# Kernel tuning notes

Hardware: AMD Instinct MI355X
Metric: run time of the kernel (lower is better)

## Reference

```python
import jax, jax.numpy as jnp
import numpy as np

N_HEADS = 16


def _apply_rope(x, cos, sin):
    # x: [B, H, S, hd]; cos/sin: [>=S, hd/2]
    S = x.shape[2]
    cos = cos[None, None, :S]
    sin = sin[None, None, :S]
    x1, x2 = x[..., ::2], x[..., 1::2]
    # interleaved rotate, matching torch stack(...).flatten(-2)
    return jnp.stack([x1 * cos - x2 * sin, x1 * sin + x2 * cos], axis=-1).reshape(x.shape)


def setup_inputs() -> dict:
    key = jax.random.key(0)
    B, S, D = 2, 2048, 1024
    hd = D // N_HEADS
    k1, k2, k3 = jax.random.split(key, 3)
    x = jax.random.normal(k1, (B, S, D), dtype=jnp.float32)
    # standard RoPE tables (theta=10000)
    inv_freq = 1.0 / (10000.0 ** (np.arange(0, hd, 2, dtype=np.float32) / hd))  # [hd/2]
    freqs = np.outer(np.arange(S, dtype=np.float32), inv_freq)  # [S, hd/2]
    rope_cos = jnp.asarray(np.cos(freqs), dtype=jnp.float32)
    rope_sin = jnp.asarray(np.sin(freqs), dtype=jnp.float32)
    W_qkv = jax.random.normal(k2, (D, 3 * D), dtype=jnp.float32) * (D ** -0.5)
    W_out = jax.random.normal(k3, (D, D), dtype=jnp.float32) * (D ** -0.5)
    return {"x": x, "rope_cos": rope_cos, "rope_sin": rope_sin, "W_qkv": W_qkv, "W_out": W_out}


def reference(x, rope_cos, rope_sin, W_qkv, W_out):
    B, S, D = x.shape
    H = N_HEADS
    hd = D // H
    qkv = (x @ W_qkv).reshape(B, S, 3, H, hd)  # fused QKV projection
    q = qkv[:, :, 0].transpose(0, 2, 1, 3)  # [B,H,S,hd]
    k = qkv[:, :, 1].transpose(0, 2, 1, 3)
    v = qkv[:, :, 2].transpose(0, 2, 1, 3)
    q = _apply_rope(q, rope_cos, rope_sin)
    k = _apply_rope(k, rope_cos, rope_sin)
    scale = hd ** -0.5
    scores = jnp.einsum('bhqd,bhkd->bhqk', q, k) * scale  # [B,H,S,S]
    causal = jnp.tril(jnp.ones((S, S), dtype=bool))
    scores = jnp.where(causal, scores, jnp.finfo(scores.dtype).min)
    attn = jax.nn.softmax(scores, axis=-1)
    out = jnp.einsum('bhqk,bhkd->bhqd', attn, v)  # [B,H,S,hd]
    out = out.transpose(0, 2, 1, 3).reshape(B, S, D)
    return out @ W_out  # dropout is identity in eval mode
```

## Files before the change

kernel.cpp:

```cpp
#include <hip/hip_runtime.h>
#include <hip/hip_bf16.h>
#include <stdint.h>

typedef short bf16x8 __attribute__((ext_vector_type(8)));
typedef short bf16x4 __attribute__((ext_vector_type(4)));
typedef float f32x4 __attribute__((ext_vector_type(4)));

#define HD 64
#define NH 16
#define SEQ 2048
#define BATCH 2
#define DM 1024
#define TOK (BATCH * SEQ)

__device__ __forceinline__ unsigned short f2bf(float f) {
    union { float f; unsigned u; } a; a.f = f;
    unsigned r = a.u + 0x7fffu + ((a.u >> 16) & 1u);
    return (unsigned short)(r >> 16);
}
__device__ __forceinline__ float bf2f(unsigned short u) {
    union { unsigned u; float f; } a; a.u = ((unsigned)u) << 16;
    return a.f;
}

__device__ __forceinline__ unsigned pkbf16(float a, float b) {
    union { __hip_bfloat162 h; unsigned u; } cv;
    cv.h = __float22bfloat162_rn(make_float2(a, b));
    return cv.u;
}

__device__ __forceinline__ float fexp2(float x) {
#if __has_builtin(__builtin_amdgcn_exp2f)
    return __builtin_amdgcn_exp2f(x);
#else
    return exp2f(x);
#endif
}
__device__ __forceinline__ float frcp(float x) {
#if __has_builtin(__builtin_amdgcn_rcpf)
    return __builtin_amdgcn_rcpf(x);
#else
    return 1.0f / x;
#endif
}

__device__ __forceinline__ f32x4 mfma16(bf16x4 a, bf16x4 b, f32x4 c) {
#if defined(__HIP_DEVICE_COMPILE__)
    return __builtin_amdgcn_mfma_f32_16x16x16bf16_1k(a, b, c, 0, 0, 0);
#else
    (void)a; (void)b;
    return c;
#endif
}

__device__ __forceinline__ void gld_lds16(const unsigned short* g, unsigned short* l) {
#if __has_builtin(__builtin_amdgcn_global_load_lds)
    __builtin_amdgcn_global_load_lds(
        (const __attribute__((address_space(1))) unsigned int*)g,
        (__attribute__((address_space(3))) unsigned int*)l, 16, 0, 0);
#else
    *(bf16x8*)l = *(const bf16x8*)g;
#endif
}

__global__ void __launch_bounds__(256) k_prep(const float* __restrict__ x,
                                              unsigned short* __restrict__ xb,
                                              const float* __restrict__ wqkv,
                                              unsigned short* __restrict__ wqkvt,
                                              const float* __restrict__ wout,
                                              unsigned short* __restrict__ woutt) {
    int bid = blockIdx.x;
    int tid = threadIdx.x;
    if (bid < 4096) {
        int i = (bid * 256 + tid) * 4;
        float4 v = *(const float4*)(x + i);
        union { ushort4 v; unsigned short s[4]; } o;
        o.s[0] = f2bf(v.x); o.s[1] = f2bf(v.y); o.s[2] = f2bf(v.z); o.s[3] = f2bf(v.w);
        *(ushort4*)(xb + i) = o.v;
        return;
    }
    const float* W; unsigned short* Wt; int N, t;
    if (bid < 7168) { W = wqkv; Wt = wqkvt; N = 3 * DM; t = bid - 4096; }
    else            { W = wout; Wt = woutt; N = DM;     t = bid - 7168; }
    int ntx = N >> 5;
    int bx = t % ntx, by = t / ntx;
    int tx = tid & 31, ty = tid >> 5;
    __shared__ float tile[32][33];
    for (int r = 0; r < 4; ++r) {
        int k = by * 32 + ty + r * 8;
        int n = bx * 32 + tx;
        tile[ty + r * 8][tx] = W[(size_t)k * N + n];
    }
    __syncthreads();
    for (int r = 0; r < 4; ++r) {
        int n = bx * 32 + ty + r * 8;
        int k = by * 32 + tx;
        Wt[(size_t)n * DM + k] = f2bf(tile[tx][ty + r * 8]);
    }
}

#define BKK 32

template <int MODE>
__device__ __forceinline__ void gemm_core(const unsigned short* __restrict__ A,
                                          const unsigned short* __restrict__ Bt,
                                          int K, int N,
                                          float* __restrict__ C,
                                          unsigned short* __restrict__ qbuf,
                                          unsigned short* __restrict__ kbuf,
                                          unsigned short* __restrict__ vt) {
    __shared__ unsigned short As0[128 * BKK];
    __shared__ unsigned short As1[128 * BKK];
    __shared__ unsigned short Bs0[128 * BKK];
    __shared__ unsigned short Bs1[128 * BKK];
    int tid = threadIdx.x;
    int lane = tid & 63, wave = tid >> 6;
    int row0 = blockIdx.y * 128;
    int col0 = blockIdx.x * 128;
    int wm = (wave >> 1) * 64, wn = (wave & 1) * 64;
    int fr = lane & 15;
    int quad = lane >> 4;

    f32x4 zero4 = {0.f, 0.f, 0.f, 0.f};
    f32x4 acc[4][4];
    for (int i = 0; i < 4; ++i)
        for (int j = 0; j < 4; ++j) acc[i][j] = zero4;

    auto stage = [&](unsigned short* Ad, unsigned short* Bd, int k0) {
        for (int i = 0; i < 2; ++i) {
            int s2 = i * 256 + tid;
            int r = s2 >> 2, kc = s2 & 3;
            int kk = (kc ^ (r & 3)) * 8;
            gld_lds16(A + (size_t)(row0 + r) * K + k0 + kk, Ad + (i * 256 + wave * 64) * 8);
            gld_lds16(Bt + (size_t)(col0 + r) * K + k0 + kk, Bd + (i * 256 + wave * 64) * 8);
        }
    };
    auto compute = [&](const unsigned short* Al, const unsigned short* Bl) {
        bf16x8 af[4], bf[4];
        for (int i = 0; i < 4; ++i) {
            int rr = wm + i * 16 + fr;
            af[i] = *(const bf16x8*)&Al[rr * BKK + ((quad ^ (rr & 3)) * 8)];
        }
        for (int j = 0; j < 4; ++j) {
            int rr = wn + j * 16 + fr;
            bf[j] = *(const bf16x8*)&Bl[rr * BKK + ((quad ^ (rr & 3)) * 8)];
        }
        for (int i = 0; i < 4; ++i)
            for (int j = 0; j < 4; ++j)
                acc[i][j] = __builtin_amdgcn_mfma_f32_16x16x32_bf16(af[i], bf[j], acc[i][j], 0, 0, 0);
    };

    stage(As0, Bs0, 0);
    __syncthreads();
    for (int k0 = 0; k0 < K; k0 += 2 * BKK) {
        if (k0 + BKK < K) stage(As1, Bs1, k0 + BKK);
        compute(As0, Bs0);
        __syncthreads();
        if (k0 + 2 * BKK < K) stage(As0, Bs0, k0 + 2 * BKK);
        compute(As1, Bs1);
        __syncthreads();
    }

    int rq = (lane >> 4) * 4;
    int cq = lane & 15;
    for (int i = 0; i < 4; ++i)
        for (int j = 0; j < 4; ++j)
            for (int reg = 0; reg < 4; ++reg) {
                int row = row0 + wm + i * 16 + rq + reg;
                int col = col0 + wn + j * 16 + cq;
                float v = acc[i][j][reg];
                if (MODE == 0) {
                    C[(size_t)row * N + col] = v;
                } else {
                    int which = col >> 10;
                    int hc = col & 1023;
                    int h = hc >> 6, d = hc & 63;
                    int b = row >> 11, s = row & (SEQ - 1);
                    int bh = b * NH + h;
                    unsigned short bv = f2bf(v);
                    if (which == 0)      qbuf[((size_t)bh * SEQ + s) * HD + d] = bv;
                    else if (which == 1) kbuf[((size_t)bh * SEQ + s) * HD + d] = bv;
                    else                 vt[((size_t)bh * HD + d) * SEQ + s] = bv;
                }
            }
}

__global__ void __launch_bounds__(256) k_gemm_qkv(const unsigned short* __restrict__ A,
                                                  const unsigned short* __restrict__ Bt,
                                                  unsigned short* __restrict__ qbuf,
                                                  unsigned short* __restrict__ kbuf,
                                                  unsigned short* __restrict__ vt) {
    gemm_core<1>(A, Bt, DM, 3 * DM, nullptr, qbuf, kbuf, vt);
}

__global__ void __launch_bounds__(256) k_gemm_out(const unsigned short* __restrict__ A,
                                                  const unsigned short* __restrict__ Bt,
                                                  float* __restrict__ C) {
    gemm_core<0>(A, Bt, DM, DM, C, nullptr, nullptr, nullptr);
}

__global__ void k_rope(unsigned short* __restrict__ qbuf, unsigned short* __restrict__ kbuf,
                       const float* __restrict__ cosb, const float* __restrict__ sinb) {
    int t = blockIdx.x * 256 + threadIdx.x;
    int c = t & 7;
    int row = (t >> 3) & 65535;
    int which = t >> 19;
    unsigned short* p = (which ? kbuf : qbuf) + (size_t)row * HD + c * 8;
    float sc = which ? 1.0f : (0.125f * 1.44269504f);
    int s = row & (SEQ - 1);
    const float* cs = cosb + s * 32 + c * 4;
    const float* sn = sinb + s * 32 + c * 4;
    bf16x8 v = *(const bf16x8*)p;
    bf16x8 o;
    for (int i = 0; i < 4; ++i) {
        float x1 = bf2f((unsigned short)v[2 * i]);
        float x2 = bf2f((unsigned short)v[2 * i + 1]);
        float cc = cs[i], ss = sn[i];
        o[2 * i]     = (short)f2bf((x1 * cc - x2 * ss) * sc);
        o[2 * i + 1] = (short)f2bf((x1 * ss + x2 * cc) * sc);
    }
    *(bf16x8*)p = o;
}

__global__ void __launch_bounds__(128, 2) k_attn(const unsigned short* __restrict__ qbuf,
                                                 const unsigned short* __restrict__ kbuf,
                                                 const unsigned short* __restrict__ vt,
                                                 unsigned short* __restrict__ obuf) {
    __shared__ unsigned short Ks0[64 * 64];
    __shared__ unsigned short Ks1[64 * 64];
    __shared__ unsigned short Vs0[64 * 64];
    __shared__ unsigned short Vs1[64 * 64];

    int tid = threadIdx.x;
    int lane = tid & 63, wave = tid >> 6;
    int bh = blockIdx.y;
    int b = bh >> 4, h = bh & 15;
    int p = ((int)blockIdx.x + (int)blockIdx.y) & 31;
    int fr = lane & 15, quad = lane >> 4, sw = fr & 7;
    int Qb0 = (2 * p + wave) * 16;
    int Qb1 = (127 - 2 * p - wave) * 16;
    int KT = ((127 - 2 * p) >> 2) + 1;

    const unsigned short* Qb = qbuf + (size_t)bh * SEQ * HD;
    const unsigned short* Kb = kbuf + (size_t)bh * SEQ * HD;
    const unsigned short* Vb = vt + (size_t)bh * HD * SEQ;

    bf16x8 qf[2][2];
    for (int s = 0; s < 2; ++s) {
        int qrow = (s ? Qb1 : Qb0) + fr;
        qf[s][0] = *(const bf16x8*)(Qb + (size_t)qrow * HD + quad * 8);
        qf[s][1] = *(const bf16x8*)(Qb + (size_t)qrow * HD + 32 + quad * 8);
    }

    f32x4 zero4 = {0.f, 0.f, 0.f, 0.f};
    f32x4 o[2][4];
    for (int s = 0; s < 2; ++s)
        for (int j = 0; j < 4; ++j) o[s][j] = zero4;
    float l[2] = {0.f, 0.f};

    auto stage = [&](int kb, unsigned short* Kd, unsigned short* Vd) {
        for (int a = 0; a < 4; ++a) {
            int idx = a * 128 + tid;
            int r = idx >> 3;
            int lg = (idx & 7) ^ (r & 7);
            gld_lds16(Kb + (size_t)(kb + r) * HD + lg * 8, Kd + (a * 128 + wave * 64) * 8);
            gld_lds16(Vb + (size_t)r * SEQ + kb + lg * 8, Vd + (a * 128 + wave * 64) * 8);
        }
    };

    auto compute = [&](int kt, const unsigned short* Kd, const unsigned short* Vd) {
        int kb = kt * 64;
        bf16x8 ka[4], kc[4];
        for (int g = 0; g < 4; ++g) {
            int r = g * 16 + fr;
            ka[g] = *(const bf16x8*)&Kd[r * 64 + ((quad ^ sw) * 8)];
            kc[g] = *(const bf16x8*)&Kd[r * 64 + (((quad + 4) ^ sw) * 8)];
        }
        bf16x4 vf[4][4];
        for (int g = 0; g < 4; ++g)
            for (int db = 0; db < 4; ++db) {
                int d = db * 16 + fr;
                int pg = ((2 * g + (quad >> 1)) ^ sw) * 8 + (quad & 1) * 4;
                vf[g][db] = *(const bf16x4*)&Vd[d * 64 + pg];
            }
        for (int s = 0; s < 2; ++s) {
            int Qs = s ? Qb1 : Qb0;
            if (kb > Qs + 15) continue;
            f32x4 sg[4];
            for (int g = 0; g < 4; ++g) {
                f32x4 z = zero4;
                z = __builtin_amdgcn_mfma_f32_16x16x32_bf16(ka[g], qf[s][0], z, 0, 0, 0);
                z = __builtin_amdgcn_mfma_f32_16x16x32_bf16(kc[g], qf[s][1], z, 0, 0, 0);
                sg[g] = z;
            }
            if (kb + 63 > Qs) {
                int q = Qs + fr;
                for (int g = 0; g < 4; ++g)
                    for (int reg = 0; reg < 4; ++reg)
                        if (kb + g * 16 + quad * 4 + reg > q) sg[g][reg] = -1e30f;
            }
            bf16x4 pf[4];
            for (int g = 0; g < 4; ++g) {
                float p0 = fexp2(sg[g][0]);
                float p1 = fexp2(sg[g][1]);
                float p2 = fexp2(sg[g][2]);
                float p3 = fexp2(sg[g][3]);
                l[s] += (p0 + p1) + (p2 + p3);
                union { bf16x4 v; unsigned u[2]; } pc;
                pc.u[0] = pkbf16(p0, p1);
                pc.u[1] = pkbf16(p2, p3);
                pf[g] = pc.v;
            }
            for (int g = 0; g < 4; ++g)
                for (int db = 0; db < 4; ++db)
                    o[s][db] = mfma16(pf[g], vf[g][db], o[s][db]);
        }
    };

    stage(0, Ks0, Vs0);
    __syncthreads();
    for (int kt = 0; kt < KT; kt += 2) {
        if (kt + 1 < KT) stage((kt + 1) * 64, Ks1, Vs1);
        compute(kt, Ks0, Vs0);
        __syncthreads();
        if (kt + 1 < KT) {
            if (kt + 2 < KT) stage((kt + 2) * 64, Ks0, Vs0);
            compute(kt + 1, Ks1, Vs1);
            __syncthreads();
        }
    }

    for (int s = 0; s < 2; ++s) {
        float ll = l[s];
        ll += __shfl_xor(ll, 16);
        ll += __shfl_xor(ll, 32);
        float linv[4];
        for (int reg = 0; reg < 4; ++reg)
            linv[reg] = frcp(__shfl(ll, quad * 4 + reg));
        int Qs = s ? Qb1 : Qb0;
        for (int db = 0; db < 4; ++db)
            for (int reg = 0; reg < 4; ++reg) {
                int row = Qs + quad * 4 + reg;
                int d = db * 16 + fr;
                obuf[((size_t)(b * SEQ + row)) * DM + h * HD + d] = f2bf(o[s][db][reg] * linv[reg]);
            }
    }
}

extern "C" void kernel_launch(void* const* d_in, const int* in_sizes, int n_in,
                              void* d_out, int out_size, void* d_ws, size_t ws_size,
                              hipStream_t stream) {
    const float* x    = (const float*)d_in[0];
    const float* rc   = (const float*)d_in[1];
    const float* rs   = (const float*)d_in[2];
    const float* wqkv = (const float*)d_in[3];
    const float* wout = (const float*)d_in[4];
    float* out = (float*)d_out;

    char* ws = (char*)d_ws;
    size_t off = 0;
    auto alloc = [&](size_t bytes) {
        char* p = ws + off;
        off += (bytes + 255) & ~(size_t)255;
        return p;
    };
    unsigned short* xb    = (unsigned short*)alloc((size_t)TOK * DM * 2);
    unsigned short* wqkvt = (unsigned short*)alloc((size_t)3 * DM * DM * 2);
    unsigned short* woutt = (unsigned short*)alloc((size_t)DM * DM * 2);
    unsigned short* qbuf  = (unsigned short*)alloc((size_t)BATCH * NH * SEQ * HD * 2);
    unsigned short* kbuf  = (unsigned short*)alloc((size_t)BATCH * NH * SEQ * HD * 2);
    unsigned short* vtb   = (unsigned short*)alloc((size_t)BATCH * NH * SEQ * HD * 2);
    unsigned short* obuf  = (unsigned short*)alloc((size_t)TOK * DM * 2);

    k_prep<<<8192, 256, 0, stream>>>(x, xb, wqkv, wqkvt, wout, woutt);
    k_gemm_qkv<<<dim3(3 * DM / 128, TOK / 128), 256, 0, stream>>>(xb, wqkvt, qbuf, kbuf, vtb);
    k_rope<<<4096, 256, 0, stream>>>(qbuf, kbuf, rc, rs);
    k_attn<<<dim3(SEQ / 64, BATCH * NH), 128, 0, stream>>>(qbuf, kbuf, vtb, obuf);
    k_gemm_out<<<dim3(DM / 128, TOK / 128), 256, 0, stream>>>(obuf, woutt, out);
}
```

Baseline: 183.4 us.

## Rewrite QKV GEMM with 256x256 tiles, triple-buffered direct-to-LDS loads and swizzled grid

Replaces the generic 128x128 QKV projection GEMM with a dedicated kernel that uses 256x256 output tiles, 512 threads (8 waves, each computing a 128x64 sub-tile) and a three-slot LDS ring fed by global-to-LDS loads with XOR-swizzled columns. Block indices are remapped so neighbouring blocks share input rows and columns in cache. MFMA issue runs at raised wave priority. The aim is more data reuse per loaded byte, loads that overlap compute, and a grid of 192 blocks that fits the CU count. The cost is higher register pressure (128 accumulator floats per lane), one block per CU, and a scattered epilogue store that is unchanged.

```diff
diff --git a/kernel.cpp b/kernel.cpp
--- a/kernel.cpp
+++ b/kernel.cpp
@@ -185,18 +185,118 @@
             }
 }
 
-__global__ void __launch_bounds__(256) k_gemm_qkv(const unsigned short* __restrict__ A,
-                                                  const unsigned short* __restrict__ Bt,
-                                                  unsigned short* __restrict__ qbuf,
-                                                  unsigned short* __restrict__ kbuf,
-                                                  unsigned short* __restrict__ vt) {
-    gemm_core<1>(A, Bt, DM, 3 * DM, nullptr, qbuf, kbuf, vt);
-}
-
 __global__ void __launch_bounds__(256) k_gemm_out(const unsigned short* __restrict__ A,
                                                   const unsigned short* __restrict__ Bt,
                                                   float* __restrict__ C) {
     gemm_core<0>(A, Bt, DM, DM, C, nullptr, nullptr, nullptr);
+}
+
+#define QBM 256
+#define QBK 32
+#define QSLOT (QBM * QBK)
+
+__global__ void __launch_bounds__(512, 1) k_gemm_qkv(const unsigned short* __restrict__ A,
+                                                     const unsigned short* __restrict__ Bt,
+                                                     unsigned short* __restrict__ qbuf,
+                                                     unsigned short* __restrict__ kbuf,
+                                                     unsigned short* __restrict__ vt) {
+    constexpr int K = DM;
+    constexpr int NT = K / QBK;
+    __shared__ __attribute__((aligned(16))) unsigned short As[3 * QSLOT];
+    __shared__ __attribute__((aligned(16))) unsigned short Bs[3 * QSLOT];
+
+    int tid = threadIdx.x;
+    int lane = tid & 63, wave = tid >> 6;
+    int wm = wave >> 2, wn = wave & 3;
+    int fr = lane & 15, quad = lane >> 4;
+
+    int lin = (int)blockIdx.x;
+    int swz = (lin & 7) * 24 + (lin >> 3);
+    int by = swz / 12, bx = swz % 12;
+    int row0 = by * 256, col0 = bx * 256;
+
+    f32x4 zero4 = {0.f, 0.f, 0.f, 0.f};
+    f32x4 acc[8][4];
+#pragma unroll
+    for (int i = 0; i < 8; ++i)
+#pragma unroll
+        for (int j = 0; j < 4; ++j) acc[i][j] = zero4;
+
+    auto stage = [&](int kt, int slot) {
+        unsigned short* Ad = As + slot * QSLOT;
+        unsigned short* Bd = Bs + slot * QSLOT;
+#pragma unroll
+        for (int a = 0; a < 2; ++a) {
+            int idx = a * 512 + tid;
+            int r = idx >> 2, c = idx & 3;
+            int kk = (c ^ ((r & 3) ^ ((r >> 2) & 3))) * 8;
+            gld_lds16(A + (size_t)(row0 + r) * K + kt * QBK + kk, Ad + (a * 512 + wave * 64) * 8);
+            gld_lds16(Bt + (size_t)(col0 + r) * K + kt * QBK + kk, Bd + (a * 512 + wave * 64) * 8);
+        }
+    };
+
+    auto body = [&](int slot, int staget, int vm) {
+        const unsigned short* Al = As + slot * QSLOT;
+        const unsigned short* Bl = Bs + slot * QSLOT;
+        bf16x8 af[8], bfr[4];
+#pragma unroll
+        for (int i = 0; i < 8; ++i) {
+            int rr = wm * 128 + i * 16 + fr;
+            af[i] = *(const bf16x8*)&Al[rr * QBK + ((quad ^ ((rr & 3) ^ ((rr >> 2) & 3))) * 8)];
+        }
+#pragma unroll
+        for (int j = 0; j < 4; ++j) {
+            int rr = wn * 64 + j * 16 + fr;
+            bfr[j] = *(const bf16x8*)&Bl[rr * QBK + ((quad ^ ((rr & 3) ^ ((rr >> 2) & 3))) * 8)];
+        }
+        asm volatile("s_waitcnt lgkmcnt(0)" ::: "memory");
+        __builtin_amdgcn_s_barrier();
+        if (staget >= 0) stage(staget, slot);
+        __builtin_amdgcn_s_setprio(1);
+#pragma unroll
+        for (int i = 0; i < 8; ++i)
+#pragma unroll
+            for (int j = 0; j < 4; ++j)
+                acc[i][j] = __builtin_amdgcn_mfma_f32_16x16x32_bf16(af[i], bfr[j], acc[i][j], 0, 0, 0);
+        __builtin_amdgcn_s_setprio(0);
+        if (vm == 8)      asm volatile("s_waitcnt vmcnt(8)" ::: "memory");
+        else if (vm == 4) asm volatile("s_waitcnt vmcnt(4)" ::: "memory");
+        else if (vm == 0) asm volatile("s_waitcnt vmcnt(0)" ::: "memory");
+        if (vm >= 0) __builtin_amdgcn_s_barrier();
+    };
+
+    stage(0, 0); stage(1, 1); stage(2, 2);
+    asm volatile("s_waitcnt vmcnt(8)" ::: "memory");
+    __builtin_amdgcn_s_barrier();
+
+    int slot = 0;
+    for (int t = 0; t + 3 < NT; ++t) {
+        body(slot, t + 3, 8);
+        slot = (slot == 2) ? 0 : slot + 1;
+    }
+    body(slot, -1, 4); slot = (slot == 2) ? 0 : slot + 1;
+    body(slot, -1, 0); slot = (slot == 2) ? 0 : slot + 1;
+    body(slot, -1, -1);
+
+    int rq = quad * 4, cq = fr;
+#pragma unroll
+    for (int i = 0; i < 8; ++i)
+#pragma unroll
+        for (int j = 0; j < 4; ++j)
+#pragma unroll
+            for (int reg = 0; reg < 4; ++reg) {
+                int row = row0 + wm * 128 + i * 16 + rq + reg;
+                int col = col0 + wn * 64 + j * 16 + cq;
+                int which = col >> 10;
+                int hc = col & 1023;
+                int h = hc >> 6, d = hc & 63;
+                int b = row >> 11, s = row & (SEQ - 1);
+                int bh = b * NH + h;
+                unsigned short bv = f2bf(acc[i][j][reg]);
+                if (which == 0)      qbuf[((size_t)bh * SEQ + s) * HD + d] = bv;
+                else if (which == 1) kbuf[((size_t)bh * SEQ + s) * HD + d] = bv;
+                else                 vt[((size_t)bh * HD + d) * SEQ + s] = bv;
+            }
 }
 
 __global__ void k_rope(unsigned short* __restrict__ qbuf, unsigned short* __restrict__ kbuf,
@@ -373,7 +473,7 @@
     unsigned short* obuf  = (unsigned short*)alloc((size_t)TOK * DM * 2);
 
     k_prep<<<8192, 256, 0, stream>>>(x, xb, wqkv, wqkvt, wout, woutt);
-    k_gemm_qkv<<<dim3(3 * DM / 128, TOK / 128), 256, 0, stream>>>(xb, wqkvt, qbuf, kbuf, vtb);
+    k_gemm_qkv<<<192, 512, 0, stream>>>(xb, wqkvt, qbuf, kbuf, vtb);
     k_rope<<<4096, 256, 0, stream>>>(qbuf, kbuf, rc, rs);
     k_attn<<<dim3(SEQ / 64, BATCH * NH), 128, 0, stream>>>(qbuf, kbuf, vtb, obuf);
     k_gemm_out<<<dim3(DM / 128, TOK / 128), 256, 0, stream>>>(obuf, woutt, out);
```

Result: slower. 207.5 us (+13.2%).
